# Kernel tuning notes

Hardware: AMD Instinct MI355X
Metric: run time of the kernel (lower is better)

The kernel has to match this reference:

```python
import jax, jax.numpy as jnp
import numpy as np

HIDDEN, HEAD_DIM, B, S = 1024, 64, 8, 2048


def setup_inputs() -> dict:
    key = jax.random.key(0)
    ks = jax.random.split(key, 8)
    scale = 1.0 / np.sqrt(HIDDEN)
    return {
        "query": jax.random.normal(ks[0], (B, S, HIDDEN), jnp.float32),
        "key": jax.random.normal(ks[1], (B, S, HIDDEN), jnp.float32),
        "value": jax.random.normal(ks[2], (B, S, HIDDEN), jnp.float32),
        "relative_biases": jax.random.normal(ks[3], (B, S, S), jnp.float32),
        "mask": jnp.ones((B, S), jnp.int32),
        "Wq": jax.random.normal(ks[4], (HEAD_DIM, HIDDEN), jnp.float32) * scale,
        "bq": jnp.zeros((HEAD_DIM,), jnp.float32),
        "Wk": jax.random.normal(ks[5], (HEAD_DIM, HIDDEN), jnp.float32) * scale,
        "bk": jnp.zeros((HEAD_DIM,), jnp.float32),
        "Wv": jax.random.normal(ks[6], (HEAD_DIM, HIDDEN), jnp.float32) * scale,
        "bv": jnp.zeros((HEAD_DIM,), jnp.float32),
    }


def reference(query, key, value, relative_biases, mask, Wq, bq, Wk, bk, Wv, bv):
    # Per-head linear projections: [B,S,H] @ [H,D] + [D]
    q = jnp.einsum("bsh,dh->bsd", query, Wq) + bq
    k = jnp.einsum("bsh,dh->bsd", key, Wk) + bk
    v = jnp.einsum("bsh,dh->bsd", value, Wv) + bv
    d = q.shape[-1]
    # (QK^T + relative_bias) / sqrt(d)  -- bias added BEFORE scaling, as in source
    scores = (jnp.einsum("bqd,bkd->bqk", q, k) + relative_biases) / jnp.sqrt(
        jnp.asarray(d, q.dtype)
    )
    # 2-D mask [B,Sk] broadcast over queries; masked_fill(mask==0, -inf)
    m = mask[:, None, :]  # [B,1,Sk]
    scores = jnp.where(m == 0, -jnp.inf, scores)
    att = jax.nn.softmax(scores, axis=-1)
    # dropout prob 0.0 (eval / identity)
    return jnp.einsum("bqk,bkd->bqd", att, v)
```

## Files before the change

kernel.cpp:

```cpp
#include <hip/hip_runtime.h>
#include <stdint.h>

typedef __bf16 bf16x4 __attribute__((ext_vector_type(4)));
typedef __bf16 bf16x8 __attribute__((ext_vector_type(8)));
typedef float  f32x4  __attribute__((ext_vector_type(4)));

#define HID 1024
#define SEQ 2048
#define NB  8

template <int AUX>
__device__ __forceinline__ void gl_lds16(const void* g, void* l) {
    __builtin_amdgcn_global_load_lds(
        (const __attribute__((address_space(1))) void*)g,
        (__attribute__((address_space(3))) void*)l, 16, 0, AUX);
}

__global__ __launch_bounds__(256) void prep_w(
    const float* __restrict__ Wq, const float* __restrict__ Wk,
    const float* __restrict__ Wv, __bf16* __restrict__ Wb)
{
    const int i = blockIdx.x * 256 + threadIdx.x;
    const int mat = i >> 14;
    const int j   = i & 16383;
    const float* src = ((mat == 0) ? Wq : (mat == 1) ? Wk : Wv) + j * 4;
    float4 f = *(const float4*)src;
    bf16x4 o = { (__bf16)f.x, (__bf16)f.y, (__bf16)f.z, (__bf16)f.w };
    *(bf16x4*)(Wb + (size_t)i * 4) = o;
}

__global__ __launch_bounds__(256, 3) void proj_kernel(
    const float* __restrict__ Xq, const float* __restrict__ Xk, const float* __restrict__ Xv,
    const __bf16* __restrict__ Wb,
    const float* __restrict__ bq_, const float* __restrict__ bk_, const float* __restrict__ bv_,
    __bf16* __restrict__ qo, __bf16* __restrict__ ko, __bf16* __restrict__ vTo)
{
    const int mat = blockIdx.y;
    const float* X   = (mat == 0) ? Xq  : (mat == 1) ? Xk  : Xv;
    const __bf16* Wm = Wb + (size_t)mat * 64 * HID;
    const float* Bp  = (mat == 0) ? bq_ : (mat == 1) ? bk_ : bv_;

    const int row0 = blockIdx.x * 64;
    const int tid  = threadIdx.x;
    const int lane = tid & 63;
    const int wv   = tid >> 6;
    const int lr   = lane & 15;
    const int g    = lane >> 4;

    __shared__ __align__(16) float  Xl[2][64 * 64];
    __shared__ __align__(16) __bf16 Wl[2][64 * 64];

    f32x4 acc[4] = {};

    auto STAGE = [&](int t, int pb) {
        const int k0 = t * 64;
        #pragma unroll
        for (int j = 0; j < 4; ++j) {
            const int row = wv * 16 + 4 * j + (lane >> 4);
            const int c   = row & 7;
            const float* src = X + (size_t)(row0 + row) * HID + k0 + 4 * ((lane & 15) ^ c);
            gl_lds16<2>(src, &Xl[pb][(wv * 16 + 4 * j) * 64]);
        }
        #pragma unroll
        for (int j = 0; j < 2; ++j) {
            const int row = wv * 16 + 8 * j + (lane >> 3);
            const int c   = row & 7;
            const __bf16* src = Wm + (size_t)row * HID + k0 + 8 * ((lane & 7) ^ c);
            gl_lds16<0>(src, &Wl[pb][(wv * 16 + 8 * j) * 64]);
        }
    };

    STAGE(0, 0);
    STAGE(1, 1);

    const int r  = wv * 16 + lr;
    const int cx = lr & 7;

    for (int t = 0; t < 16; ++t) {
        const int pb = t & 1;
        if (t < 15) { asm volatile("s_waitcnt vmcnt(6)" ::: "memory"); }
        else        { asm volatile("s_waitcnt vmcnt(0)" ::: "memory"); }
        __builtin_amdgcn_s_barrier();

        #pragma unroll
        for (int kk = 0; kk < 2; ++kk) {
            const int ulo = 2 * g + 8 * kk;
            f32x4 xa = *(const f32x4*)&Xl[pb][r * 64 + (((ulo)     ^ cx) << 2)];
            f32x4 xb = *(const f32x4*)&Xl[pb][r * 64 + (((ulo + 1) ^ cx) << 2)];
            bf16x8 af = { (__bf16)xa.x, (__bf16)xa.y, (__bf16)xa.z, (__bf16)xa.w,
                          (__bf16)xb.x, (__bf16)xb.y, (__bf16)xb.z, (__bf16)xb.w };
            #pragma unroll
            for (int ct = 0; ct < 4; ++ct) {
                const int uw = g + 4 * kk;
                bf16x8 bf = *(const bf16x8*)&Wl[pb][(ct * 16 + lr) * 64 + ((uw ^ cx) << 3)];
                acc[ct] = __builtin_amdgcn_mfma_f32_16x16x32_bf16(af, bf, acc[ct], 0, 0, 0);
            }
        }

        __builtin_amdgcn_s_barrier();
        if (t + 2 < 16) STAGE(t + 2, pb);
    }

    const float scl = (mat == 0) ? 0.125f : 1.0f;
    float res[4][4];
    #pragma unroll
    for (int ct = 0; ct < 4; ++ct) {
        const float bval = Bp[ct * 16 + lr];
        #pragma unroll
        for (int rr = 0; rr < 4; ++rr) res[ct][rr] = (acc[ct][rr] + bval) * scl;
    }

    if (mat < 2) {
        __bf16* o = (mat == 0) ? qo : ko;
        #pragma unroll
        for (int ct = 0; ct < 4; ++ct)
            #pragma unroll
            for (int rr = 0; rr < 4; ++rr)
                o[(size_t)(row0 + wv * 16 + 4 * g + rr) * 64 + ct * 16 + lr] = (__bf16)res[ct][rr];
    } else {
        __bf16* Tl = (__bf16*)&Xl[0][0];
        __syncthreads();
        #pragma unroll
        for (int ct = 0; ct < 4; ++ct)
            #pragma unroll
            for (int rr = 0; rr < 4; ++rr)
                Tl[(ct * 16 + lr) * 72 + wv * 16 + 4 * g + rr] = (__bf16)res[ct][rr];
        __syncthreads();
        const int d   = tid >> 2;
        const int sc_ = (tid & 3) * 16;
        const int b   = row0 >> 11;
        const int s0  = row0 & 2047;
        __bf16* dst = vTo + ((size_t)b * 64 + d) * SEQ + s0 + sc_;
        *(bf16x8*)dst       = *(const bf16x8*)&Tl[d * 72 + sc_];
        *(bf16x8*)(dst + 8) = *(const bf16x8*)&Tl[d * 72 + sc_ + 8];
    }
}

__global__ __launch_bounds__(128) void attn_kernel(
    const __bf16* __restrict__ qws, const __bf16* __restrict__ kws,
    const __bf16* __restrict__ vTws, const float* __restrict__ bias,
    const int* __restrict__ mask, float* __restrict__ out)
{
    const int bid = blockIdx.x;
    const int b   = bid & 7;
    const int q0  = (bid >> 3) * 32;
    const int tid = threadIdx.x;
    const int lane = tid & 63;
    const int wv   = tid >> 6;
    const int lr   = lane & 15;
    const int g    = lane >> 4;

    __shared__ __align__(16) __bf16 Kl[64 * 72];
    __shared__ __align__(16) __bf16 Vl[64 * 72];

    const int qrow = q0 + wv * 16 + lr;

    bf16x8 qf[2];
    {
        const __bf16* qp = qws + (size_t)(b * SEQ + qrow) * 64;
        #pragma unroll
        for (int dt = 0; dt < 2; ++dt) {
            bf16x4 lo = *(const bf16x4*)(qp + dt * 32 + 4 * g);
            bf16x4 hi = *(const bf16x4*)(qp + dt * 32 + 16 + 4 * g);
            qf[dt] = __builtin_shufflevector(lo, hi, 0, 1, 2, 3, 4, 5, 6, 7);
        }
    }

    f32x4 O[4] = {};
    float m   = -3.0e38f;
    float ell = 0.0f;

    const float* brow = bias + (size_t)(b * SEQ + qrow) * SEQ;
    const int*   mrow = mask + b * SEQ;

    const int sr = tid >> 1;
    const int sc = (tid & 1) * 32;
    const __bf16* kbase = kws  + (size_t)(b * SEQ + sr) * 64 + sc;
    const __bf16* vbase = vTws + ((size_t)b * 64 + sr) * SEQ + sc;

    bf16x8 kr[4], vr[4];
    float4 bvn[4]; int4 mkn[4];

    auto loadt = [&](int kt) {
        const __bf16* ks = kbase + (size_t)kt * 64;
        kr[0] = *(const bf16x8*)ks;
        kr[1] = *(const bf16x8*)(ks + 8);
        kr[2] = *(const bf16x8*)(ks + 16);
        kr[3] = *(const bf16x8*)(ks + 24);
        const __bf16* vs = vbase + kt;
        vr[0] = *(const bf16x8*)vs;
        vr[1] = *(const bf16x8*)(vs + 8);
        vr[2] = *(const bf16x8*)(vs + 16);
        vr[3] = *(const bf16x8*)(vs + 24);
        #pragma unroll
        for (int s2t = 0; s2t < 4; ++s2t) {
            bvn[s2t] = *(const float4*)(brow + kt + s2t * 16 + 4 * g);
            mkn[s2t] = *(const int4*)(mrow + kt + s2t * 16 + 4 * g);
        }
    };

    loadt(0);

    #pragma unroll 2
    for (int kt = 0; kt < SEQ; kt += 64) {
        *(bf16x8*)&Kl[sr * 72 + sc]      = kr[0];
        *(bf16x8*)&Kl[sr * 72 + sc + 8]  = kr[1];
        *(bf16x8*)&Kl[sr * 72 + sc + 16] = kr[2];
        *(bf16x8*)&Kl[sr * 72 + sc + 24] = kr[3];
        *(bf16x8*)&Vl[sr * 72 + sc]      = vr[0];
        *(bf16x8*)&Vl[sr * 72 + sc + 8]  = vr[1];
        *(bf16x8*)&Vl[sr * 72 + sc + 16] = vr[2];
        *(bf16x8*)&Vl[sr * 72 + sc + 24] = vr[3];
        float4 bv4[4]; int4 mk4[4];
        #pragma unroll
        for (int s2t = 0; s2t < 4; ++s2t) { bv4[s2t] = bvn[s2t]; mk4[s2t] = mkn[s2t]; }
        __syncthreads();

        if (kt + 64 < SEQ) loadt(kt + 64);

        float p[16];
        #pragma unroll
        for (int s2t = 0; s2t < 4; ++s2t) {
            const int s2 = s2t * 16;
            f32x4 acc = {};
            #pragma unroll
            for (int dt = 0; dt < 2; ++dt) {
                bf16x4 klo = *(const bf16x4*)&Kl[(s2 + lr) * 72 + dt * 32 + 4 * g];
                bf16x4 khi = *(const bf16x4*)&Kl[(s2 + lr) * 72 + dt * 32 + 16 + 4 * g];
                bf16x8 kf = __builtin_shufflevector(klo, khi, 0, 1, 2, 3, 4, 5, 6, 7);
                acc = __builtin_amdgcn_mfma_f32_16x16x32_bf16(kf, qf[dt], acc, 0, 0, 0);
            }
            p[s2t * 4 + 0] = mk4[s2t].x ? acc[0] + 0.125f * bv4[s2t].x : -1e30f;
            p[s2t * 4 + 1] = mk4[s2t].y ? acc[1] + 0.125f * bv4[s2t].y : -1e30f;
            p[s2t * 4 + 2] = mk4[s2t].z ? acc[2] + 0.125f * bv4[s2t].z : -1e30f;
            p[s2t * 4 + 3] = mk4[s2t].w ? acc[3] + 0.125f * bv4[s2t].w : -1e30f;
        }

        float tmax = p[0];
        #pragma unroll
        for (int i = 1; i < 16; ++i) tmax = fmaxf(tmax, p[i]);
        tmax = fmaxf(tmax, __shfl_xor(tmax, 16));
        tmax = fmaxf(tmax, __shfl_xor(tmax, 32));
        const float mnew  = fmaxf(m, tmax);
        const float scale = __expf(m - mnew);
        m = mnew;
        float ssum = 0.0f;
        #pragma unroll
        for (int i = 0; i < 16; ++i) { p[i] = __expf(p[i] - mnew); ssum += p[i]; }
        ssum += __shfl_xor(ssum, 16);
        ssum += __shfl_xor(ssum, 32);
        ell = ell * scale + ssum;

        float scr[4];
        #pragma unroll
        for (int rr = 0; rr < 4; ++rr) scr[rr] = __shfl(scale, 4 * g + rr);
        #pragma unroll
        for (int t = 0; t < 4; ++t)
            #pragma unroll
            for (int rr = 0; rr < 4; ++rr) O[t][rr] *= scr[rr];

        bf16x8 pf0 = { (__bf16)p[0],  (__bf16)p[1],  (__bf16)p[2],  (__bf16)p[3],
                       (__bf16)p[4],  (__bf16)p[5],  (__bf16)p[6],  (__bf16)p[7] };
        bf16x8 pf1 = { (__bf16)p[8],  (__bf16)p[9],  (__bf16)p[10], (__bf16)p[11],
                       (__bf16)p[12], (__bf16)p[13], (__bf16)p[14], (__bf16)p[15] };

        #pragma unroll
        for (int t = 0; t < 4; ++t) {
            const int dr = (t * 16 + lr) * 72;
            bf16x4 v0lo = *(const bf16x4*)&Vl[dr + 4 * g];
            bf16x4 v0hi = *(const bf16x4*)&Vl[dr + 16 + 4 * g];
            bf16x8 vf0 = __builtin_shufflevector(v0lo, v0hi, 0, 1, 2, 3, 4, 5, 6, 7);
            O[t] = __builtin_amdgcn_mfma_f32_16x16x32_bf16(pf0, vf0, O[t], 0, 0, 0);
            bf16x4 v1lo = *(const bf16x4*)&Vl[dr + 32 + 4 * g];
            bf16x4 v1hi = *(const bf16x4*)&Vl[dr + 48 + 4 * g];
            bf16x8 vf1 = __builtin_shufflevector(v1lo, v1hi, 0, 1, 2, 3, 4, 5, 6, 7);
            O[t] = __builtin_amdgcn_mfma_f32_16x16x32_bf16(pf1, vf1, O[t], 0, 0, 0);
        }
        __syncthreads();
    }

    float linv[4];
    #pragma unroll
    for (int rr = 0; rr < 4; ++rr) linv[rr] = 1.0f / __shfl(ell, 4 * g + rr);

    float* orow = out + (size_t)(b * SEQ + q0 + wv * 16) * 64;
    #pragma unroll
    for (int t = 0; t < 4; ++t)
        #pragma unroll
        for (int rr = 0; rr < 4; ++rr)
            orow[(size_t)(4 * g + rr) * 64 + t * 16 + lr] = O[t][rr] * linv[rr];
}

extern "C" void kernel_launch(void* const* d_in, const int* in_sizes, int n_in,
                              void* d_out, int out_size, void* d_ws, size_t ws_size,
                              hipStream_t stream) {
    const float* query = (const float*)d_in[0];
    const float* key_  = (const float*)d_in[1];
    const float* value = (const float*)d_in[2];
    const float* rb    = (const float*)d_in[3];
    const int*   mask  = (const int*)d_in[4];
    const float* Wq = (const float*)d_in[5];
    const float* bq = (const float*)d_in[6];
    const float* Wk = (const float*)d_in[7];
    const float* bk = (const float*)d_in[8];
    const float* Wv = (const float*)d_in[9];
    const float* bv = (const float*)d_in[10];

    __bf16* qws = (__bf16*)d_ws;
    __bf16* kws = qws + (size_t)16384 * 64;
    __bf16* vT  = kws + (size_t)16384 * 64;
    __bf16* Wbf = vT  + (size_t)8 * 64 * SEQ;

    hipLaunchKernelGGL(prep_w, dim3(192), dim3(256), 0, stream, Wq, Wk, Wv, Wbf);
    hipLaunchKernelGGL(proj_kernel, dim3(256, 3), dim3(256), 0, stream,
                       query, key_, value, Wbf, bq, bk, bv, qws, kws, vT);
    hipLaunchKernelGGL(attn_kernel, dim3(512), dim3(128), 0, stream,
                       qws, kws, vT, rb, mask, (float*)d_out);
}
```

Before: 92.09 us.

## Split projection GEMM along K into two halves with separate reduce kernel

The projection kernel now splits the 1024-wide hidden reduction into two halves across a new grid dimension, doubling block count (1536 blocks) and halving LDS tiles so more blocks fit per CU. Partial fp32 results go to a workspace, and a new reduce kernel sums them, adds bias and scale, and writes q/k and transposed v in bf16. This targets the low block count of the memory-bound projection, at the cost of an extra kernel launch and an extra write and read of the fp32 partials.

```diff
diff --git a/kernel.cpp b/kernel.cpp
--- a/kernel.cpp
+++ b/kernel.cpp
@@ -29,16 +29,14 @@
     *(bf16x4*)(Wb + (size_t)i * 4) = o;
 }
 
-__global__ __launch_bounds__(256, 3) void proj_kernel(
+__global__ __launch_bounds__(256, 6) void proj_kernel(
     const float* __restrict__ Xq, const float* __restrict__ Xk, const float* __restrict__ Xv,
-    const __bf16* __restrict__ Wb,
-    const float* __restrict__ bq_, const float* __restrict__ bk_, const float* __restrict__ bv_,
-    __bf16* __restrict__ qo, __bf16* __restrict__ ko, __bf16* __restrict__ vTo)
+    const __bf16* __restrict__ Wb, float* __restrict__ Pw)
 {
     const int mat = blockIdx.y;
+    const int h   = blockIdx.z;
     const float* X   = (mat == 0) ? Xq  : (mat == 1) ? Xk  : Xv;
     const __bf16* Wm = Wb + (size_t)mat * 64 * HID;
-    const float* Bp  = (mat == 0) ? bq_ : (mat == 1) ? bk_ : bv_;
 
     const int row0 = blockIdx.x * 64;
     const int tid  = threadIdx.x;
@@ -47,26 +45,26 @@
     const int lr   = lane & 15;
     const int g    = lane >> 4;
 
-    __shared__ __align__(16) float  Xl[2][64 * 64];
-    __shared__ __align__(16) __bf16 Wl[2][64 * 64];
+    __shared__ __align__(16) float  Xl[2][64 * 32];
+    __shared__ __align__(16) __bf16 Wl[2][64 * 32];
 
     f32x4 acc[4] = {};
+    const int kbase = h * 512;
 
     auto STAGE = [&](int t, int pb) {
-        const int k0 = t * 64;
-        #pragma unroll
-        for (int j = 0; j < 4; ++j) {
-            const int row = wv * 16 + 4 * j + (lane >> 4);
-            const int c   = row & 7;
-            const float* src = X + (size_t)(row0 + row) * HID + k0 + 4 * ((lane & 15) ^ c);
-            gl_lds16<2>(src, &Xl[pb][(wv * 16 + 4 * j) * 64]);
-        }
+        const int k0 = kbase + t * 32;
         #pragma unroll
         for (int j = 0; j < 2; ++j) {
             const int row = wv * 16 + 8 * j + (lane >> 3);
-            const int c   = row & 7;
-            const __bf16* src = Wm + (size_t)row * HID + k0 + 8 * ((lane & 7) ^ c);
-            gl_lds16<0>(src, &Wl[pb][(wv * 16 + 8 * j) * 64]);
+            const float* src = X + (size_t)(row0 + row) * HID + k0
+                             + 4 * ((lane & 7) ^ (row & 7));
+            gl_lds16<2>(src, &Xl[pb][(wv * 16 + 8 * j) * 32]);
+        }
+        {
+            const int row = wv * 16 + (lane >> 2);
+            const __bf16* src = Wm + (size_t)row * HID + k0
+                              + 8 * ((lane & 3) ^ (row & 3));
+            gl_lds16<0>(src, &Wl[pb][(wv * 16) * 32]);
         }
     };
 
@@ -75,56 +73,77 @@
 
     const int r  = wv * 16 + lr;
     const int cx = lr & 7;
+    const int cw = lr & 3;
 
     for (int t = 0; t < 16; ++t) {
         const int pb = t & 1;
-        if (t < 15) { asm volatile("s_waitcnt vmcnt(6)" ::: "memory"); }
+        if (t < 15) { asm volatile("s_waitcnt vmcnt(3)" ::: "memory"); }
         else        { asm volatile("s_waitcnt vmcnt(0)" ::: "memory"); }
         __builtin_amdgcn_s_barrier();
 
-        #pragma unroll
-        for (int kk = 0; kk < 2; ++kk) {
-            const int ulo = 2 * g + 8 * kk;
-            f32x4 xa = *(const f32x4*)&Xl[pb][r * 64 + (((ulo)     ^ cx) << 2)];
-            f32x4 xb = *(const f32x4*)&Xl[pb][r * 64 + (((ulo + 1) ^ cx) << 2)];
-            bf16x8 af = { (__bf16)xa.x, (__bf16)xa.y, (__bf16)xa.z, (__bf16)xa.w,
-                          (__bf16)xb.x, (__bf16)xb.y, (__bf16)xb.z, (__bf16)xb.w };
-            #pragma unroll
-            for (int ct = 0; ct < 4; ++ct) {
-                const int uw = g + 4 * kk;
-                bf16x8 bf = *(const bf16x8*)&Wl[pb][(ct * 16 + lr) * 64 + ((uw ^ cx) << 3)];
-                acc[ct] = __builtin_amdgcn_mfma_f32_16x16x32_bf16(af, bf, acc[ct], 0, 0, 0);
-            }
+        f32x4 xa = *(const f32x4*)&Xl[pb][r * 32 + (((2 * g)     ^ cx) << 2)];
+        f32x4 xb = *(const f32x4*)&Xl[pb][r * 32 + (((2 * g + 1) ^ cx) << 2)];
+        bf16x8 af = { (__bf16)xa.x, (__bf16)xa.y, (__bf16)xa.z, (__bf16)xa.w,
+                      (__bf16)xb.x, (__bf16)xb.y, (__bf16)xb.z, (__bf16)xb.w };
+        #pragma unroll
+        for (int ct = 0; ct < 4; ++ct) {
+            bf16x8 bf = *(const bf16x8*)&Wl[pb][(ct * 16 + lr) * 32 + ((g ^ cw) << 3)];
+            acc[ct] = __builtin_amdgcn_mfma_f32_16x16x32_bf16(af, bf, acc[ct], 0, 0, 0);
         }
 
         __builtin_amdgcn_s_barrier();
         if (t + 2 < 16) STAGE(t + 2, pb);
     }
 
+    float* P = Pw + ((size_t)(h * 3 + mat) * 16384 + row0) * 64;
+    #pragma unroll
+    for (int ct = 0; ct < 4; ++ct)
+        #pragma unroll
+        for (int rr = 0; rr < 4; ++rr)
+            P[(wv * 16 + 4 * g + rr) * 64 + ct * 16 + lr] = acc[ct][rr];
+}
+
+__global__ __launch_bounds__(256) void reduce_kernel(
+    const float* __restrict__ Pw,
+    const float* __restrict__ bq_, const float* __restrict__ bk_, const float* __restrict__ bv_,
+    __bf16* __restrict__ qo, __bf16* __restrict__ ko, __bf16* __restrict__ vTo)
+{
+    const int mat  = blockIdx.y;
+    const int row0 = blockIdx.x * 64;
+    const float* Bp = (mat == 0) ? bq_ : (mat == 1) ? bk_ : bv_;
     const float scl = (mat == 0) ? 0.125f : 1.0f;
-    float res[4][4];
+
+    const int tid = threadIdx.x;
+    const int r   = tid >> 2;
+    const int c4  = (tid & 3) * 16;
+
+    const float* P0 = Pw + ((size_t)(0 * 3 + mat) * 16384 + row0 + r) * 64 + c4;
+    const float* P1 = Pw + ((size_t)(1 * 3 + mat) * 16384 + row0 + r) * 64 + c4;
+
+    float res[16];
     #pragma unroll
-    for (int ct = 0; ct < 4; ++ct) {
-        const float bval = Bp[ct * 16 + lr];
-        #pragma unroll
-        for (int rr = 0; rr < 4; ++rr) res[ct][rr] = (acc[ct][rr] + bval) * scl;
+    for (int q4 = 0; q4 < 4; ++q4) {
+        f32x4 a = *(const f32x4*)(P0 + q4 * 4);
+        f32x4 b = *(const f32x4*)(P1 + q4 * 4);
+        #pragma unroll
+        for (int i = 0; i < 4; ++i)
+            res[q4 * 4 + i] = (a[i] + b[i] + Bp[c4 + q4 * 4 + i]) * scl;
     }
 
     if (mat < 2) {
         __bf16* o = (mat == 0) ? qo : ko;
-        #pragma unroll
-        for (int ct = 0; ct < 4; ++ct)
-            #pragma unroll
-            for (int rr = 0; rr < 4; ++rr)
-                o[(size_t)(row0 + wv * 16 + 4 * g + rr) * 64 + ct * 16 + lr] = (__bf16)res[ct][rr];
+        bf16x8 v0 = { (__bf16)res[0], (__bf16)res[1], (__bf16)res[2], (__bf16)res[3],
+                      (__bf16)res[4], (__bf16)res[5], (__bf16)res[6], (__bf16)res[7] };
+        bf16x8 v1 = { (__bf16)res[8],  (__bf16)res[9],  (__bf16)res[10], (__bf16)res[11],
+                      (__bf16)res[12], (__bf16)res[13], (__bf16)res[14], (__bf16)res[15] };
+        __bf16* dst = o + (size_t)(row0 + r) * 64 + c4;
+        *(bf16x8*)dst       = v0;
+        *(bf16x8*)(dst + 8) = v1;
     } else {
-        __bf16* Tl = (__bf16*)&Xl[0][0];
-        __syncthreads();
-        #pragma unroll
-        for (int ct = 0; ct < 4; ++ct)
-            #pragma unroll
-            for (int rr = 0; rr < 4; ++rr)
-                Tl[(ct * 16 + lr) * 72 + wv * 16 + 4 * g + rr] = (__bf16)res[ct][rr];
+        __shared__ __align__(16) __bf16 Tl[64 * 72];
+        #pragma unroll
+        for (int i = 0; i < 16; ++i)
+            Tl[(c4 + i) * 72 + r] = (__bf16)res[i];
         __syncthreads();
         const int d   = tid >> 2;
         const int sc_ = (tid & 3) * 16;
@@ -310,10 +329,13 @@
     __bf16* kws = qws + (size_t)16384 * 64;
     __bf16* vT  = kws + (size_t)16384 * 64;
     __bf16* Wbf = vT  + (size_t)8 * 64 * SEQ;
+    float*  Pw  = (float*)(Wbf + (size_t)3 * 64 * HID);
 
     hipLaunchKernelGGL(prep_w, dim3(192), dim3(256), 0, stream, Wq, Wk, Wv, Wbf);
-    hipLaunchKernelGGL(proj_kernel, dim3(256, 3), dim3(256), 0, stream,
-                       query, key_, value, Wbf, bq, bk, bv, qws, kws, vT);
+    hipLaunchKernelGGL(proj_kernel, dim3(256, 3, 2), dim3(256), 0, stream,
+                       query, key_, value, Wbf, Pw);
+    hipLaunchKernelGGL(reduce_kernel, dim3(256, 3), dim3(256), 0, stream,
+                       Pw, bq, bk, bv, qws, kws, vT);
     hipLaunchKernelGGL(attn_kernel, dim3(512), dim3(128), 0, stream,
                        qws, kws, vT, rb, mask, (float*)d_out);
 }
```

New measurement: 107.1 us. +16.3%, slower.

## Double-buffer register prefetch of K/V/bias tiles two iterations ahead

Applied to the files above, without the earlier changes.

Keeps two register stages of K, V, bias and mask tiles and prefetches each one two iterations ahead instead of one, alternating stages in a manually unrolled loop. A sched_barrier after each prefetch keeps the compiler from moving the loads. The goal is to hide more global-memory latency, chiefly from the large bias stream. It doubles the prefetch register footprint, which may lower occupancy or cause spills.

```diff
diff --git a/kernel.cpp b/kernel.cpp
--- a/kernel.cpp
+++ b/kernel.cpp
@@ -135,6 +135,12 @@
         *(bf16x8*)(dst + 8) = *(const bf16x8*)&Tl[d * 72 + sc_ + 8];
     }
 }
+
+struct KVStage {
+    bf16x8 kr[4], vr[4];
+    float4 bvn[4];
+    int4   mkn[4];
+};
 
 __global__ __launch_bounds__(128) void attn_kernel(
     const __bf16* __restrict__ qws, const __bf16* __restrict__ kws,
@@ -178,45 +184,42 @@
     const __bf16* kbase = kws  + (size_t)(b * SEQ + sr) * 64 + sc;
     const __bf16* vbase = vTws + ((size_t)b * 64 + sr) * SEQ + sc;
 
-    bf16x8 kr[4], vr[4];
-    float4 bvn[4]; int4 mkn[4];
-
-    auto loadt = [&](int kt) {
+    KVStage S0, S1;
+
+    auto loadt = [&](KVStage& S, int kt) {
         const __bf16* ks = kbase + (size_t)kt * 64;
-        kr[0] = *(const bf16x8*)ks;
-        kr[1] = *(const bf16x8*)(ks + 8);
-        kr[2] = *(const bf16x8*)(ks + 16);
-        kr[3] = *(const bf16x8*)(ks + 24);
+        S.kr[0] = *(const bf16x8*)ks;
+        S.kr[1] = *(const bf16x8*)(ks + 8);
+        S.kr[2] = *(const bf16x8*)(ks + 16);
+        S.kr[3] = *(const bf16x8*)(ks + 24);
         const __bf16* vs = vbase + kt;
-        vr[0] = *(const bf16x8*)vs;
-        vr[1] = *(const bf16x8*)(vs + 8);
-        vr[2] = *(const bf16x8*)(vs + 16);
-        vr[3] = *(const bf16x8*)(vs + 24);
+        S.vr[0] = *(const bf16x8*)vs;
+        S.vr[1] = *(const bf16x8*)(vs + 8);
+        S.vr[2] = *(const bf16x8*)(vs + 16);
+        S.vr[3] = *(const bf16x8*)(vs + 24);
         #pragma unroll
         for (int s2t = 0; s2t < 4; ++s2t) {
-            bvn[s2t] = *(const float4*)(brow + kt + s2t * 16 + 4 * g);
-            mkn[s2t] = *(const int4*)(mrow + kt + s2t * 16 + 4 * g);
-        }
+            S.bvn[s2t] = *(const float4*)(brow + kt + s2t * 16 + 4 * g);
+            S.mkn[s2t] = *(const int4*)(mrow + kt + s2t * 16 + 4 * g);
+        }
+        __builtin_amdgcn_sched_barrier(0);
     };
 
-    loadt(0);
-
-    #pragma unroll 2
-    for (int kt = 0; kt < SEQ; kt += 64) {
-        *(bf16x8*)&Kl[sr * 72 + sc]      = kr[0];
-        *(bf16x8*)&Kl[sr * 72 + sc + 8]  = kr[1];
-        *(bf16x8*)&Kl[sr * 72 + sc + 16] = kr[2];
-        *(bf16x8*)&Kl[sr * 72 + sc + 24] = kr[3];
-        *(bf16x8*)&Vl[sr * 72 + sc]      = vr[0];
-        *(bf16x8*)&Vl[sr * 72 + sc + 8]  = vr[1];
-        *(bf16x8*)&Vl[sr * 72 + sc + 16] = vr[2];
-        *(bf16x8*)&Vl[sr * 72 + sc + 24] = vr[3];
+    auto ITER = [&](KVStage& S, int kt) {
+        *(bf16x8*)&Kl[sr * 72 + sc]      = S.kr[0];
+        *(bf16x8*)&Kl[sr * 72 + sc + 8]  = S.kr[1];
+        *(bf16x8*)&Kl[sr * 72 + sc + 16] = S.kr[2];
+        *(bf16x8*)&Kl[sr * 72 + sc + 24] = S.kr[3];
+        *(bf16x8*)&Vl[sr * 72 + sc]      = S.vr[0];
+        *(bf16x8*)&Vl[sr * 72 + sc + 8]  = S.vr[1];
+        *(bf16x8*)&Vl[sr * 72 + sc + 16] = S.vr[2];
+        *(bf16x8*)&Vl[sr * 72 + sc + 24] = S.vr[3];
         float4 bv4[4]; int4 mk4[4];
         #pragma unroll
-        for (int s2t = 0; s2t < 4; ++s2t) { bv4[s2t] = bvn[s2t]; mk4[s2t] = mkn[s2t]; }
+        for (int s2t = 0; s2t < 4; ++s2t) { bv4[s2t] = S.bvn[s2t]; mk4[s2t] = S.mkn[s2t]; }
         __syncthreads();
 
-        if (kt + 64 < SEQ) loadt(kt + 64);
+        if (kt + 128 < SEQ) loadt(S, kt + 128);
 
         float p[16];
         #pragma unroll
@@ -277,6 +280,15 @@
             O[t] = __builtin_amdgcn_mfma_f32_16x16x32_bf16(pf1, vf1, O[t], 0, 0, 0);
         }
         __syncthreads();
+    };
+
+    loadt(S0, 0);
+    loadt(S1, 64);
+
+    #pragma unroll 1
+    for (int kt = 0; kt < SEQ; kt += 128) {
+        ITER(S0, kt);
+        ITER(S1, kt + 64);
     }
 
     float linv[4];
```

Measured after the change: 105.4 us. +14.4%, slower.
